# Kernel optimization log

Hardware: AMD Instinct MI355X
Metric: run time of the kernel (lower is better)

The kernel has to match this reference:

```python
import jax, jax.numpy as jnp
import numpy as np

B, CIN, COUT, K, S = 4, 16, 16, 3, 64  # batch, in/out channels, kernel, spatial edge


def setup_inputs() -> dict:
    key = jax.random.key(0)
    k1, k2, k3 = jax.random.split(key, 3)
    x = jax.random.normal(k1, (B, CIN, S, S, S), dtype=jnp.float32)
    # kaiming-uniform-like scale for a 3x3x3 conv weight
    fan_in = CIN * K * K * K
    bound = 1.0 / np.sqrt(fan_in)
    weight = jax.random.uniform(k2, (COUT, CIN, K, K, K), dtype=jnp.float32,
                                minval=-bound, maxval=bound)
    bias = jax.random.uniform(k3, (COUT,), dtype=jnp.float32,
                              minval=-bound, maxval=bound)
    return {"x": x, "weight": weight, "bias": bias}


def reference(x, weight, bias):
    # ConvNd forward: N=3, stride=1, padding=1, dilation=1, groups=1.
    # Output shape [B, COUT, S, S, S] ('same' spatial sizes).
    out = jax.lax.conv_general_dilated(
        x, weight,
        window_strides=(1, 1, 1),
        padding=[(1, 1)] * 3,
        rhs_dilation=(1, 1, 1),
        dimension_numbers=("NCDHW", "OIDHW", "NCDHW"),
        feature_group_count=1,
    )
    return out + bias[None, :, None, None, None]
```

## Files before the change

### kernel.cpp

```cpp
#include <hip/hip_runtime.h>
#include <hip/hip_bf16.h>

#define S 64
#define BATCH 4
#define SH 66
#define PLANE_USH (SH * SH * 16)
#define XT_USH ((size_t)SH * PLANE_USH)
#define XT_B (XT_USH * 2)
#define XT_TOTAL (XT_B * BATCH)
#define NPAIR 14

typedef short bf16x8 __attribute__((ext_vector_type(8)));
typedef float f32x4 __attribute__((ext_vector_type(4)));

__global__ __launch_bounds__(256) void prep_wf(const float* __restrict__ w,
                                               ushort* __restrict__ wf) {
    for (int e = threadIdx.x; e < NPAIR * 64 * 8; e += 256) {
        int p = e >> 9, l = (e >> 3) & 63, j = e & 7;
        int k = ((l >> 4) << 3) + j;
        int tap = 2 * p + (k >> 4);
        int cin = k & 15, cout = l & 15;
        float v = (tap < 27) ? w[(cout * 16 + cin) * 27 + tap] : 0.0f;
        __hip_bfloat16 hb = __float2bfloat16(v);
        wf[e] = *reinterpret_cast<ushort*>(&hb);
    }
}

__global__ __launch_bounds__(256) void xform(const float* __restrict__ x,
                                             ushort* __restrict__ xt) {
    __shared__ ushort tl[4][64][18];
    const int zp = blockIdx.x;
    const int yseg = blockIdx.y;
    const int b = blockIdx.z;
    const int t = threadIdx.x;
    ushort* xtb = xt + (size_t)b * XT_USH;
    ushort* plane = xtb + (size_t)zp * PLANE_USH;

    if (zp == 0 || zp == SH - 1) {
        uint4* p4 = reinterpret_cast<uint4*>(plane);
        for (int i = yseg * 2178 + t; i < (yseg + 1) * 2178; i += 256)
            p4[i] = uint4{0, 0, 0, 0};
        return;
    }
    const int z = zp - 1;
    if (yseg == 0) {
        uint4* p4 = reinterpret_cast<uint4*>(plane);
        if (t < 132) p4[t] = uint4{0, 0, 0, 0};
    } else if (yseg == 3) {
        uint4* p4 = reinterpret_cast<uint4*>(plane + 65 * SH * 16);
        if (t < 132) p4[t] = uint4{0, 0, 0, 0};
    }

    const int r = t >> 6, xx = t & 63;
    for (int yq = 0; yq < 4; ++yq) {
        const int y = yseg * 16 + yq * 4;
        __syncthreads();
        #pragma unroll
        for (int cin = 0; cin < 16; ++cin) {
            float v = x[(((size_t)(b * 16 + cin) * S + z) * S + (y + r)) * S + xx];
            __hip_bfloat16 hb = __float2bfloat16(v);
            tl[r][xx][cin] = *reinterpret_cast<ushort*>(&hb);
        }
        __syncthreads();
        #pragma unroll
        for (int rr = 0; rr < 4; ++rr) {
            ushort* row = plane + (size_t)(y + rr + 1) * (SH * 16);
            const int xs = t >> 2, cs = (t & 3) * 4;
            uint v0 = *reinterpret_cast<const uint*>(&tl[rr][xs][cs]);
            uint v1 = *reinterpret_cast<const uint*>(&tl[rr][xs][cs + 2]);
            uint* dp = reinterpret_cast<uint*>(row + 16 + t * 4);
            dp[0] = v0; dp[1] = v1;
            if (t == 0) {
                uint4* h = reinterpret_cast<uint4*>(row);
                h[0] = uint4{0, 0, 0, 0}; h[1] = uint4{0, 0, 0, 0};
            } else if (t == 1) {
                uint4* h = reinterpret_cast<uint4*>(row + 65 * 16);
                h[0] = uint4{0, 0, 0, 0}; h[1] = uint4{0, 0, 0, 0};
            }
        }
    }
}

__global__ __launch_bounds__(256) void conv_mfma(const ushort* __restrict__ xt,
                                                 const ushort* __restrict__ wf,
                                                 const float* __restrict__ bias,
                                                 float* __restrict__ out) {
    const int t = threadIdx.x;
    const int lane = t & 63, w = t >> 6;
    const int hi = lane >> 4, lo = lane & 15;
    const int y = blockIdx.x * 4 + w, z = blockIdx.y, b = blockIdx.z;

    bf16x8 bfr[NPAIR];
    #pragma unroll
    for (int p = 0; p < NPAIR; ++p)
        bfr[p] = *reinterpret_cast<const bf16x8*>(wf + ((size_t)p * 64 + lane) * 8);

    const char* xtb = reinterpret_cast<const char*>(xt) + (size_t)b * XT_B;
    const char* zerop = xtb + lane * 16;
    const char* base0 = xtb + ((size_t)(z * SH + y) * SH + lo) * 32 + (hi & 1) * 16;

    const float bv = bias[lo];
    f32x4 acc[4];
    #pragma unroll
    for (int g = 0; g < 4; ++g) acc[g] = {bv, bv, bv, bv};

    #pragma unroll
    for (int p = 0; p < NPAIR; ++p) {
        const int t0 = 2 * p, t1 = 2 * p + 1;
        const int o0 = (((t0 / 9) * SH + (t0 % 9) / 3) * SH + (t0 % 3)) * 32;
        const int o1 = (t1 < 27) ? (((t1 / 9) * SH + (t1 % 9) / 3) * SH + (t1 % 3)) * 32 : 0;
        const int osel = (hi < 2) ? o0 : o1;
        const bool zsel = (hi >= 2) && (t1 >= 27);
        #pragma unroll
        for (int g = 0; g < 4; ++g) {
            const char* pa = zsel ? zerop : (base0 + g * (16 * 32) + osel);
            bf16x8 af = *reinterpret_cast<const bf16x8*>(pa);
            acc[g] = __builtin_amdgcn_mfma_f32_16x16x32_bf16(af, bfr[p], acc[g], 0, 0, 0);
        }
    }

    __shared__ float osh[4][64][17];
    #pragma unroll
    for (int g = 0; g < 4; ++g)
        #pragma unroll
        for (int j = 0; j < 4; ++j)
            osh[w][g * 16 + hi * 4 + j][lo] = acc[g][j];
    __syncthreads();
    const int cout = t >> 4, xs = (t & 15) * 4;
    #pragma unroll
    for (int ww = 0; ww < 4; ++ww) {
        float4 o = make_float4(osh[ww][xs][cout], osh[ww][xs + 1][cout],
                               osh[ww][xs + 2][cout], osh[ww][xs + 3][cout]);
        *reinterpret_cast<float4*>(
            out + ((((size_t)b * 16 + cout) * S + z) * S + (blockIdx.x * 4 + ww)) * S + xs) = o;
    }
}

extern "C" void kernel_launch(void* const* d_in, const int* in_sizes, int n_in,
                              void* d_out, int out_size, void* d_ws, size_t ws_size,
                              hipStream_t stream)
{
    (void)in_sizes; (void)n_in; (void)out_size; (void)ws_size;
    const float* x    = (const float*)d_in[0];
    const float* w    = (const float*)d_in[1];
    const float* bias = (const float*)d_in[2];
    float* out        = (float*)d_out;

    ushort* xt = (ushort*)d_ws;
    ushort* wf = (ushort*)((char*)d_ws + XT_TOTAL);

    prep_wf<<<1, 256, 0, stream>>>(w, wf);
    xform<<<dim3(SH, 4, BATCH), 256, 0, stream>>>(x, xt);
    conv_mfma<<<dim3(16, S, BATCH), 256, 0, stream>>>(xt, wf, bias, out);
}
```

Baseline: 158.8 us.

## Stage input slab in LDS for conv MFMA and vectorize transform loads

The conv kernel now cooperatively copies the three padded z-planes (6 rows each) it needs into shared memory, then reads its MFMA A-fragments from LDS instead of issuing repeated global loads for every tap. The padding tap is redirected to a duplicated real tap with zero weights, and the output staging buffer reuses the same LDS. The transform kernel uses float4 loads over a finer grid with one sync per block, and weight prep is spread over 28 blocks. This trades a larger LDS footprint, which may lower occupancy, for fewer redundant global/L2 reads.

```diff
diff --git a/kernel.cpp b/kernel.cpp
--- a/kernel.cpp
+++ b/kernel.cpp
@@ -4,127 +4,145 @@
 #define S 64
 #define BATCH 4
 #define SH 66
-#define PLANE_USH (SH * SH * 16)
-#define XT_USH ((size_t)SH * PLANE_USH)
-#define XT_B (XT_USH * 2)
+#define ROW_B 2112
+#define PLANE_B ((size_t)SH * ROW_B)
+#define XT_B ((size_t)SH * PLANE_B)
 #define XT_TOTAL (XT_B * BATCH)
 #define NPAIR 14
+#define SLAB_P 12672
 
 typedef short bf16x8 __attribute__((ext_vector_type(8)));
 typedef float f32x4 __attribute__((ext_vector_type(4)));
 
 __global__ __launch_bounds__(256) void prep_wf(const float* __restrict__ w,
                                                ushort* __restrict__ wf) {
-    for (int e = threadIdx.x; e < NPAIR * 64 * 8; e += 256) {
-        int p = e >> 9, l = (e >> 3) & 63, j = e & 7;
-        int k = ((l >> 4) << 3) + j;
-        int tap = 2 * p + (k >> 4);
-        int cin = k & 15, cout = l & 15;
-        float v = (tap < 27) ? w[(cout * 16 + cin) * 27 + tap] : 0.0f;
-        __hip_bfloat16 hb = __float2bfloat16(v);
-        wf[e] = *reinterpret_cast<ushort*>(&hb);
-    }
+    int e = blockIdx.x * 256 + threadIdx.x;
+    int p = e >> 9, l = (e >> 3) & 63, j = e & 7;
+    int k = ((l >> 4) << 3) + j;
+    int tap = 2 * p + (k >> 4);
+    int cin = k & 15, cout = l & 15;
+    float v = (tap < 27) ? w[(cout * 16 + cin) * 27 + tap] : 0.0f;
+    __hip_bfloat16 hb = __float2bfloat16(v);
+    wf[e] = *reinterpret_cast<ushort*>(&hb);
 }
 
 __global__ __launch_bounds__(256) void xform(const float* __restrict__ x,
-                                             ushort* __restrict__ xt) {
+                                             char* __restrict__ xt) {
     __shared__ ushort tl[4][64][18];
-    const int zp = blockIdx.x;
-    const int yseg = blockIdx.y;
-    const int b = blockIdx.z;
+    const int zp = blockIdx.x, yq = blockIdx.y, b = blockIdx.z;
     const int t = threadIdx.x;
-    ushort* xtb = xt + (size_t)b * XT_USH;
-    ushort* plane = xtb + (size_t)zp * PLANE_USH;
+    char* xtb = xt + (size_t)b * XT_B;
+    char* plane = xtb + (size_t)zp * PLANE_B;
 
     if (zp == 0 || zp == SH - 1) {
         uint4* p4 = reinterpret_cast<uint4*>(plane);
-        for (int i = yseg * 2178 + t; i < (yseg + 1) * 2178; i += 256)
+        for (int i = yq * 256 + t; i < (int)(PLANE_B / 16); i += 4096)
             p4[i] = uint4{0, 0, 0, 0};
         return;
     }
     const int z = zp - 1;
-    if (yseg == 0) {
+    const int y0 = yq * 4;
+    const int cin = t >> 4, xq = t & 15;
+
+    float4 v[4];
+    #pragma unroll
+    for (int i = 0; i < 4; ++i)
+        v[i] = *reinterpret_cast<const float4*>(
+            x + (((size_t)(b * 16 + cin) * S + z) * S + (y0 + i)) * S + xq * 4);
+    #pragma unroll
+    for (int i = 0; i < 4; ++i) {
+        #pragma unroll
+        for (int u = 0; u < 4; ++u) {
+            float f = (u == 0) ? v[i].x : (u == 1) ? v[i].y : (u == 2) ? v[i].z : v[i].w;
+            __hip_bfloat16 hb = __float2bfloat16(f);
+            tl[i][xq * 4 + u][cin] = *reinterpret_cast<ushort*>(&hb);
+        }
+    }
+    __syncthreads();
+
+    const int xx = t >> 2, c4 = (t & 3) * 4;
+    #pragma unroll
+    for (int i = 0; i < 4; ++i) {
+        char* row = plane + (size_t)(y0 + i + 1) * ROW_B;
+        uint a = *reinterpret_cast<const uint*>(&tl[i][xx][c4]);
+        uint bq = *reinterpret_cast<const uint*>(&tl[i][xx][c4 + 2]);
+        uint2 val = {a, bq};
+        *reinterpret_cast<uint2*>(row + 32 + t * 8) = val;
+        if (t == 0) {
+            uint4 zz4 = {0, 0, 0, 0};
+            reinterpret_cast<uint4*>(row)[0] = zz4;
+            reinterpret_cast<uint4*>(row)[1] = zz4;
+        } else if (t == 1) {
+            uint4 zz4 = {0, 0, 0, 0};
+            reinterpret_cast<uint4*>(row + 65 * 32)[0] = zz4;
+            reinterpret_cast<uint4*>(row + 65 * 32)[1] = zz4;
+        }
+    }
+    if (yq == 0) {
         uint4* p4 = reinterpret_cast<uint4*>(plane);
         if (t < 132) p4[t] = uint4{0, 0, 0, 0};
-    } else if (yseg == 3) {
-        uint4* p4 = reinterpret_cast<uint4*>(plane + 65 * SH * 16);
+    } else if (yq == 15) {
+        uint4* p4 = reinterpret_cast<uint4*>(plane + 65 * ROW_B);
         if (t < 132) p4[t] = uint4{0, 0, 0, 0};
-    }
-
-    const int r = t >> 6, xx = t & 63;
-    for (int yq = 0; yq < 4; ++yq) {
-        const int y = yseg * 16 + yq * 4;
-        __syncthreads();
-        #pragma unroll
-        for (int cin = 0; cin < 16; ++cin) {
-            float v = x[(((size_t)(b * 16 + cin) * S + z) * S + (y + r)) * S + xx];
-            __hip_bfloat16 hb = __float2bfloat16(v);
-            tl[r][xx][cin] = *reinterpret_cast<ushort*>(&hb);
-        }
-        __syncthreads();
-        #pragma unroll
-        for (int rr = 0; rr < 4; ++rr) {
-            ushort* row = plane + (size_t)(y + rr + 1) * (SH * 16);
-            const int xs = t >> 2, cs = (t & 3) * 4;
-            uint v0 = *reinterpret_cast<const uint*>(&tl[rr][xs][cs]);
-            uint v1 = *reinterpret_cast<const uint*>(&tl[rr][xs][cs + 2]);
-            uint* dp = reinterpret_cast<uint*>(row + 16 + t * 4);
-            dp[0] = v0; dp[1] = v1;
-            if (t == 0) {
-                uint4* h = reinterpret_cast<uint4*>(row);
-                h[0] = uint4{0, 0, 0, 0}; h[1] = uint4{0, 0, 0, 0};
-            } else if (t == 1) {
-                uint4* h = reinterpret_cast<uint4*>(row + 65 * 16);
-                h[0] = uint4{0, 0, 0, 0}; h[1] = uint4{0, 0, 0, 0};
-            }
-        }
     }
 }
 
-__global__ __launch_bounds__(256) void conv_mfma(const ushort* __restrict__ xt,
+__global__ __launch_bounds__(256) void conv_mfma(const char* __restrict__ xt,
                                                  const ushort* __restrict__ wf,
                                                  const float* __restrict__ bias,
                                                  float* __restrict__ out) {
-    const int t = threadIdx.x;
-    const int lane = t & 63, w = t >> 6;
+    __shared__ char slab[3 * SLAB_P];
+    const int t = threadIdx.x, lane = t & 63, wid = t >> 6;
     const int hi = lane >> 4, lo = lane & 15;
-    const int y = blockIdx.x * 4 + w, z = blockIdx.y, b = blockIdx.z;
+    const int y0 = blockIdx.x * 4, z0 = blockIdx.y, b = blockIdx.z;
+    const char* xtb = xt + (size_t)b * XT_B;
 
     bf16x8 bfr[NPAIR];
     #pragma unroll
     for (int p = 0; p < NPAIR; ++p)
         bfr[p] = *reinterpret_cast<const bf16x8*>(wf + ((size_t)p * 64 + lane) * 8);
 
-    const char* xtb = reinterpret_cast<const char*>(xt) + (size_t)b * XT_B;
-    const char* zerop = xtb + lane * 16;
-    const char* base0 = xtb + ((size_t)(z * SH + y) * SH + lo) * 32 + (hi & 1) * 16;
+    #pragma unroll
+    for (int p = 0; p < 3; ++p) {
+        const char* gsrc = xtb + ((size_t)(z0 + p) * SH + y0) * ROW_B;
+        #pragma unroll
+        for (int i = 0; i < 4; ++i) {
+            int idx = i * 256 + t;
+            if (idx < SLAB_P / 16) {
+                uint4 val = *reinterpret_cast<const uint4*>(gsrc + idx * 16);
+                *reinterpret_cast<uint4*>(slab + p * SLAB_P + idx * 16) = val;
+            }
+        }
+    }
 
     const float bv = bias[lo];
     f32x4 acc[4];
     #pragma unroll
     for (int g = 0; g < 4; ++g) acc[g] = {bv, bv, bv, bv};
 
+    __syncthreads();
+
     #pragma unroll
     for (int p = 0; p < NPAIR; ++p) {
-        const int t0 = 2 * p, t1 = 2 * p + 1;
-        const int o0 = (((t0 / 9) * SH + (t0 % 9) / 3) * SH + (t0 % 3)) * 32;
-        const int o1 = (t1 < 27) ? (((t1 / 9) * SH + (t1 % 9) / 3) * SH + (t1 % 3)) * 32 : 0;
-        const int osel = (hi < 2) ? o0 : o1;
-        const bool zsel = (hi >= 2) && (t1 >= 27);
+        const int t0 = 2 * p;
+        const int t1 = (2 * p + 1 < 27) ? 2 * p + 1 : 26;
+        const int o0 = (t0 / 9) * SLAB_P + ((t0 / 3) % 3 + wid) * ROW_B + (lo + t0 % 3) * 32;
+        const int o1 = (t1 / 9) * SLAB_P + ((t1 / 3) % 3 + wid) * ROW_B + (lo + t1 % 3) * 32;
+        const int sel = ((hi < 2) ? o0 : o1) + ((hi & 1) << 4);
         #pragma unroll
         for (int g = 0; g < 4; ++g) {
-            const char* pa = zsel ? zerop : (base0 + g * (16 * 32) + osel);
-            bf16x8 af = *reinterpret_cast<const bf16x8*>(pa);
+            bf16x8 af = *reinterpret_cast<const bf16x8*>(slab + sel + g * 512);
             acc[g] = __builtin_amdgcn_mfma_f32_16x16x32_bf16(af, bfr[p], acc[g], 0, 0, 0);
         }
     }
 
-    __shared__ float osh[4][64][17];
+    __syncthreads();
+    float (*osh)[64][17] = reinterpret_cast<float (*)[64][17]>(slab);
     #pragma unroll
     for (int g = 0; g < 4; ++g)
         #pragma unroll
         for (int j = 0; j < 4; ++j)
-            osh[w][g * 16 + hi * 4 + j][lo] = acc[g][j];
+            osh[wid][g * 16 + hi * 4 + j][lo] = acc[g][j];
     __syncthreads();
     const int cout = t >> 4, xs = (t & 15) * 4;
     #pragma unroll
@@ -132,7 +150,7 @@
         float4 o = make_float4(osh[ww][xs][cout], osh[ww][xs + 1][cout],
                                osh[ww][xs + 2][cout], osh[ww][xs + 3][cout]);
         *reinterpret_cast<float4*>(
-            out + ((((size_t)b * 16 + cout) * S + z) * S + (blockIdx.x * 4 + ww)) * S + xs) = o;
+            out + ((((size_t)b * 16 + cout) * S + z0) * S + (y0 + ww)) * S + xs) = o;
     }
 }
 
@@ -146,10 +164,10 @@
     const float* bias = (const float*)d_in[2];
     float* out        = (float*)d_out;
 
-    ushort* xt = (ushort*)d_ws;
+    char* xt   = (char*)d_ws;
     ushort* wf = (ushort*)((char*)d_ws + XT_TOTAL);
 
-    prep_wf<<<1, 256, 0, stream>>>(w, wf);
-    xform<<<dim3(SH, 4, BATCH), 256, 0, stream>>>(x, xt);
+    prep_wf<<<28, 256, 0, stream>>>(w, wf);
+    xform<<<dim3(SH, 16, BATCH), 256, 0, stream>>>(x, xt);
     conv_mfma<<<dim3(16, S, BATCH), 256, 0, stream>>>(xt, wf, bias, out);
 }
```

Result: faster. 142.7 us (-10.1%).
